# Kernel tuning notes

Measured on AMD Instinct MI355X. Metric: run time of the kernel, lower is better.

## Reference

```python
import jax, jax.numpy as jnp
import numpy as np

HIDDEN = 1024
FEAT = 64
BATCH = 512
SEQ = 64
EPS = 1e-5


def _gru_layer(x_seq, Wih, Whh, bih, bhh):
    # x_seq: [B,T,Din]; Wih: [3H,Din]; Whh: [3H,H]; gate order r,z,n (PyTorch)
    B = x_seq.shape[0]
    H = Whh.shape[1]
    gates_x = jnp.einsum('btd,gd->btg', x_seq, Wih) + bih  # [B,T,3H]
    h0 = jnp.zeros((B, H), x_seq.dtype)

    def step(h, gx):
        gh = h @ Whh.T + bhh                       # [B,3H]
        xr, xz, xn = jnp.split(gx, 3, axis=-1)
        hr, hz, hn = jnp.split(gh, 3, axis=-1)
        r = jax.nn.sigmoid(xr + hr)
        z = jax.nn.sigmoid(xz + hz)
        n = jnp.tanh(xn + r * hn)
        h_new = (1.0 - z) * n + z * h
        return h_new, h_new

    _, ys = jax.lax.scan(step, h0, jnp.swapaxes(gates_x, 0, 1))  # [T,B,H]
    return jnp.swapaxes(ys, 0, 1)                                # [B,T,H]


def setup_inputs() -> dict:
    key = jax.random.key(0)
    ks = jax.random.split(key, 20)
    s = 1.0 / np.sqrt(HIDDEN)
    u = lambda k, shape: jax.random.uniform(k, shape, jnp.float32, -s, s)
    inp = {
        'x': jax.random.normal(ks[0], (BATCH, SEQ, FEAT), jnp.float32),
        'Wih0': u(ks[1], (3 * HIDDEN, FEAT)),
        'Whh0': u(ks[2], (3 * HIDDEN, HIDDEN)),
        'bih0': u(ks[3], (3 * HIDDEN,)),
        'bhh0': u(ks[4], (3 * HIDDEN,)),
        'Wih1': u(ks[5], (3 * HIDDEN, HIDDEN)),
        'Whh1': u(ks[6], (3 * HIDDEN, HIDDEN)),
        'bih1': u(ks[7], (3 * HIDDEN,)),
        'bhh1': u(ks[8], (3 * HIDDEN,)),
        'Wih2': u(ks[9], (3 * HIDDEN, HIDDEN)),
        'Whh2': u(ks[10], (3 * HIDDEN, HIDDEN)),
        'bih2': u(ks[11], (3 * HIDDEN,)),
        'bhh2': u(ks[12], (3 * HIDDEN,)),
        'gamma': jnp.ones((HIDDEN,), jnp.float32),
        'beta': jnp.zeros((HIDDEN,), jnp.float32),
        'fcW': u(ks[13], (1, HIDDEN)),
        'fcb': u(ks[14], (1,)),
    }
    return inp


def reference(x, Wih0, Whh0, bih0, bhh0, Wih1, Whh1, bih1, bhh1,
              Wih2, Whh2, bih2, bhh2, gamma, beta, fcW, fcb):
    h = _gru_layer(x, Wih0, Whh0, bih0, bhh0)
    h = _gru_layer(h, Wih1, Whh1, bih1, bhh1)
    h = _gru_layer(h, Wih2, Whh2, bih2, bhh2)
    out = h[:, -1, :]                               # [B,H] last timestep
    # BatchNorm1d in training mode: biased batch stats (B != 1 branch)
    mu = jnp.mean(out, axis=0)
    var = jnp.mean((out - mu) ** 2, axis=0)
    out = (out - mu) * jax.lax.rsqrt(var + EPS) * gamma + beta
    out = out @ fcW.T + fcb                         # [B,1]
    return jax.nn.sigmoid(out)[:, 0]                # [B]
```

## Files before the change

kernel.cpp:

```cpp
#include <hip/hip_runtime.h>
#include <hip/hip_bf16.h>
#include <stdint.h>

#define HIDDEN 1024
#define FEAT   64
#define BATCH  512
#define SEQ    64
#define GATES  3072

typedef __attribute__((ext_vector_type(4))) float f32x4;
typedef __attribute__((ext_vector_type(8))) short s16x8;

#define MFMA16(a, b, c) __builtin_amdgcn_mfma_f32_16x16x32_bf16(a, b, c, 0, 0, 0)
#define VMCNT(n) asm volatile("s_waitcnt vmcnt(" #n ")" ::: "memory")
#define LGKMCNT0 asm volatile("s_waitcnt lgkmcnt(0)" ::: "memory")

__device__ inline unsigned short f2bf(float f) {
    unsigned u = __builtin_bit_cast(unsigned, f);
    u += 0x7fff + ((u >> 16) & 1);
    return (unsigned short)(u >> 16);
}
__device__ inline float bf2f(unsigned short s) {
    unsigned u = ((unsigned)s) << 16;
    return __builtin_bit_cast(float, u);
}

#define GLOAD_LDS16(g, l) __builtin_amdgcn_global_load_lds( \
    (const __attribute__((address_space(1))) unsigned int*)(g), \
    (__attribute__((address_space(3))) unsigned int*)(l), 16, 0, 0)

__global__ void k_conv_whh(const float* __restrict__ src, unsigned short* __restrict__ dst) {
    int i = blockIdx.x * 256 + threadIdx.x;
    int d = i >> 10, k = i & 1023;
    int ub = d / 48, rem = d - ub * 48;
    int g = rem >> 4, jj = rem & 15;
    int srow = g * 1024 + ub * 16 + jj;
    dst[i] = f2bf(src[(size_t)srow * 1024 + k]);
}

__global__ void k_conv_wih0(const float* __restrict__ src, unsigned short* __restrict__ dst) {
    int i = blockIdx.x * 256 + threadIdx.x;
    int d = i >> 6, k = i & 63;
    int ub = d / 48, rem = d - ub * 48;
    int g = rem >> 4, jj = rem & 15;
    int srow = g * 1024 + ub * 16 + jj;
    dst[i] = f2bf(src[(size_t)srow * 64 + k]);
}

__global__ void k_xpose(const float* __restrict__ x, unsigned short* __restrict__ xbf) {
    int i = blockIdx.x * blockDim.x + threadIdx.x;
    if (i >= BATCH * SEQ * FEAT) return;
    int f = i & 63, t = (i >> 6) & 63, b = i >> 12;
    xbf[((size_t)t * BATCH + b) * FEAT + f] = f2bf(x[i]);
}

__device__ __forceinline__ void stage_pair(const char* ws, int wstr, const char* as, int astr,
                                           unsigned short* Wd, unsigned short* Ad,
                                           int wid, int lane)
{
    const int lrow = lane >> 3;
    const int lcol = lane & 7;
    for (int g = wid; g < 6; g += 4) {
        int row = g * 8 + lrow;
        int c16 = lcol ^ (row & 7);
        GLOAD_LDS16(ws + (size_t)row * wstr + c16 * 16, (char*)Wd + (g << 10));
    }
#pragma unroll
    for (int r = 0; r < 4; ++r) {
        int g = wid + r * 4;
        int row = g * 8 + lrow;
        int c16 = lcol ^ (row & 7);
        GLOAD_LDS16(as + (size_t)row * astr + c16 * 16, (char*)Ad + (g << 10));
    }
}

template<int NSLOT>
__device__ __forceinline__ void compute_chunk(const unsigned short* aL, const unsigned short* wL,
                                              int wid, int lane, f32x4 (&acc)[2][4])
{
    const int l15 = lane & 15, hi = lane >> 4;
    const int swz = (l15 & 7) << 4;
    const char* ap = (const char*)aL;
    const char* wp = (const char*)wL;
#pragma unroll
    for (int ks = 0; ks < 2; ++ks) {
        const int kb = ks * 64 + (hi << 4);
        s16x8 a0 = *(const s16x8*)(ap + ((((wid * 32 + l15) * 128) + kb) ^ swz));
        s16x8 a1 = *(const s16x8*)(ap + ((((wid * 32 + 16 + l15) * 128) + kb) ^ swz));
        s16x8 b0 = *(const s16x8*)(wp + (((l15 * 128) + kb) ^ swz));
        s16x8 b1 = *(const s16x8*)(wp + ((((16 + l15) * 128) + kb) ^ swz));
        s16x8 b2 = *(const s16x8*)(wp + ((((32 + l15) * 128) + kb) ^ swz));
        acc[0][0]     = MFMA16(a0, b0, acc[0][0]);
        acc[0][1]     = MFMA16(a0, b1, acc[0][1]);
        acc[0][NSLOT] = MFMA16(a0, b2, acc[0][NSLOT]);
        acc[1][0]     = MFMA16(a1, b0, acc[1][0]);
        acc[1][1]     = MFMA16(a1, b1, acc[1][1]);
        acc[1][NSLOT] = MFMA16(a1, b2, acc[1][NSLOT]);
    }
}

__global__ __launch_bounds__(256, 3) void k_stage(
    int d,
    const unsigned short* __restrict__ xbf,
    unsigned short* __restrict__ h0,
    unsigned short* __restrict__ h1,
    unsigned short* __restrict__ h2,
    const unsigned short* __restrict__ wih0R,
    const unsigned short* __restrict__ whh0R,
    const unsigned short* __restrict__ wih1R,
    const unsigned short* __restrict__ whh1R,
    const unsigned short* __restrict__ wih2R,
    const unsigned short* __restrict__ whh2R,
    const float* __restrict__ bih0, const float* __restrict__ bhh0,
    const float* __restrict__ bih1, const float* __restrict__ bhh1,
    const float* __restrict__ bih2, const float* __restrict__ bhh2)
{
    __shared__ unsigned short Wb[2][48 * 64];
    __shared__ unsigned short Ab[2][128 * 64];
    const int bid = blockIdx.x;
    const int slot = bid & 7;
    const int p = (bid >> 3) % 24;
    const int bg = bid / 192;
    const int pair = slot + 8 * p;
    const int layer = pair >> 6;
    const int ub = pair & 63;
    const int t = d - layer;
    if (t < 0 || t >= SEQ) return;

    const int tid = threadIdx.x;
    const int wid = tid >> 6, lane = tid & 63;
    const int l15 = lane & 15, hi = lane >> 4;
    const int brow0 = bg * 128;

    const unsigned short* inseq = (layer == 0) ? xbf : ((layer == 1) ? h0 : h1);
    unsigned short* outseq = (layer == 0) ? h0 : ((layer == 1) ? h1 : h2);
    const unsigned short* wihR = (layer == 0) ? wih0R : ((layer == 1) ? wih1R : wih2R);
    const unsigned short* whhR = (layer == 0) ? whh0R : ((layer == 1) ? whh1R : whh2R);

    const int astr1 = (layer == 0) ? 128 : 2048;
    const char* a1base = (layer == 0)
        ? (const char*)xbf + (size_t)t * BATCH * FEAT * 2 + (size_t)brow0 * 128
        : (const char*)inseq + (size_t)t * BATCH * HIDDEN * 2 + (size_t)brow0 * 2048;
    const char* w1base = (layer == 0)
        ? (const char*)wihR + (size_t)ub * 48 * 64 * 2
        : (const char*)wihR + (size_t)ub * 48 * 1024 * 2;
    const int wstr1 = (layer == 0) ? 128 : 2048;
    const char* a2base = (const char*)outseq + (size_t)(t - 1) * BATCH * HIDDEN * 2 + (size_t)brow0 * 2048;
    const char* w2base = (const char*)whhR + (size_t)ub * 48 * 1024 * 2;

    const int NCH1 = (layer == 0) ? 1 : 16;
    const int NCH2 = (t > 0) ? 16 : 0;
    const int total = NCH1 + NCH2;

    auto srcs = [&](int c, const char*& ws, int& wstr, const char*& as, int& astr) {
        if (c < NCH1) {
            ws = w1base + (size_t)c * 128; wstr = wstr1;
            as = a1base + (size_t)c * 128; astr = astr1;
        } else {
            int c2 = c - NCH1;
            ws = w2base + (size_t)c2 * 128; wstr = 2048;
            as = a2base + (size_t)c2 * 128; astr = 2048;
        }
    };

    f32x4 acc[2][4];
    const f32x4 zero = {0.f, 0.f, 0.f, 0.f};
#pragma unroll
    for (int i = 0; i < 2; ++i)
#pragma unroll
        for (int s = 0; s < 4; ++s) acc[i][s] = zero;

    {
        const char* ws; int wstr; const char* as; int astr;
        srcs(0, ws, wstr, as, astr);
        stage_pair(ws, wstr, as, astr, Wb[0], Ab[0], wid, lane);
    }

    for (int c = 0; c < total; ++c) {
        const int cb = c & 1;
        if (c + 1 < total) {
            const char* ws; int wstr; const char* as; int astr;
            srcs(c + 1, ws, wstr, as, astr);
            stage_pair(ws, wstr, as, astr, Wb[cb ^ 1], Ab[cb ^ 1], wid, lane);
            if (wid < 2) VMCNT(6); else VMCNT(5);
        } else {
            VMCNT(0);
        }
        __builtin_amdgcn_s_barrier();
        __builtin_amdgcn_sched_barrier(0);
        if (c < NCH1) compute_chunk<2>(Ab[cb], Wb[cb], wid, lane, acc);
        else          compute_chunk<3>(Ab[cb], Wb[cb], wid, lane, acc);
        LGKMCNT0;
        __builtin_amdgcn_sched_barrier(0);
        __builtin_amdgcn_s_barrier();
    }

    const float* bih = (layer == 0) ? bih0 : ((layer == 1) ? bih1 : bih2);
    const float* bhh = (layer == 0) ? bhh0 : ((layer == 1) ? bhh1 : bhh2);
    const int j = ub * 16 + l15;
    const float br  = bih[j] + bhh[j];
    const float bz  = bih[HIDDEN + j] + bhh[HIDDEN + j];
    const float bxn = bih[2 * HIDDEN + j];
    const float bhn = bhh[2 * HIDDEN + j];
    const unsigned short* hprev = outseq + (size_t)((t > 0) ? (t - 1) : 0) * (BATCH * HIDDEN);
    unsigned short* hout = outseq + (size_t)t * (BATCH * HIDDEN);
#pragma unroll
    for (int i = 0; i < 2; ++i)
#pragma unroll
        for (int r = 0; r < 4; ++r) {
            int brow = brow0 + wid * 32 + i * 16 + hi * 4 + r;
            size_t hidx = (size_t)brow * HIDDEN + j;
            float rg = 1.f / (1.f + __expf(-(acc[i][0][r] + br)));
            float zg = 1.f / (1.f + __expf(-(acc[i][1][r] + bz)));
            float ng = tanhf(acc[i][2][r] + bxn + rg * (acc[i][3][r] + bhn));
            float hv = (t > 0) ? bf2f(hprev[hidx]) : 0.f;
            float hnew = (1.f - zg) * ng + zg * hv;
            hout[hidx] = f2bf(hnew);
        }
}

__global__ void k_bn_part(const unsigned short* __restrict__ h, float* __restrict__ part) {
    int j = threadIdx.x;
    int blk = blockIdx.x;
    float s = 0.f, q = 0.f;
    for (int b = blk * 32; b < blk * 32 + 32; ++b) {
        float v = bf2f(h[(size_t)b * HIDDEN + j]);
        s += v; q += v * v;
    }
    part[blk * 2048 + j] = s;
    part[blk * 2048 + 1024 + j] = q;
}

__global__ void k_bn_fold(const float* __restrict__ part, const float* __restrict__ gamma,
                          const float* __restrict__ beta, float* __restrict__ a, float* __restrict__ bb)
{
    int j = blockIdx.x * 256 + threadIdx.x;
    float s = 0.f, q = 0.f;
    for (int p = 0; p < 16; ++p) {
        s += part[p * 2048 + j];
        q += part[p * 2048 + 1024 + j];
    }
    float mu = s * (1.f / BATCH);
    float var = q * (1.f / BATCH) - mu * mu;
    float rs = rsqrtf(var + 1e-5f);
    float aj = gamma[j] * rs;
    a[j] = aj;
    bb[j] = beta[j] - mu * aj;
}

__global__ void k_fc(const unsigned short* __restrict__ h, const float* __restrict__ a, const float* __restrict__ bb,
                     const float* __restrict__ fcW, const float* __restrict__ fcb, float* __restrict__ out)
{
    int b = blockIdx.x;
    int lane = threadIdx.x;
    float s = 0.f;
    for (int j = lane; j < HIDDEN; j += 64)
        s += (bf2f(h[(size_t)b * HIDDEN + j]) * a[j] + bb[j]) * fcW[j];
#pragma unroll
    for (int m = 32; m; m >>= 1) s += __shfl_xor(s, m, 64);
    if (lane == 0) out[b] = 1.f / (1.f + __expf(-(s + fcb[0])));
}

extern "C" void kernel_launch(void* const* d_in, const int* in_sizes, int n_in,
                              void* d_out, int out_size, void* d_ws, size_t ws_size,
                              hipStream_t stream)
{
    const float* x = (const float*)d_in[0];
    const float* W_ih[3] = {(const float*)d_in[1], (const float*)d_in[5], (const float*)d_in[9]};
    const float* W_hh[3] = {(const float*)d_in[2], (const float*)d_in[6], (const float*)d_in[10]};
    const float* b_ih[3] = {(const float*)d_in[3], (const float*)d_in[7], (const float*)d_in[11]};
    const float* b_hh[3] = {(const float*)d_in[4], (const float*)d_in[8], (const float*)d_in[12]};
    const float* gamma = (const float*)d_in[13];
    const float* beta  = (const float*)d_in[14];
    const float* fcW   = (const float*)d_in[15];
    const float* fcb   = (const float*)d_in[16];

    char* ws = (char*)d_ws;
    size_t off = 0;
    auto alloc = [&](size_t bytes) -> void* {
        void* p = ws + off;
        off = (off + bytes + 255) & ~(size_t)255;
        return p;
    };
    unsigned short* wih0R = (unsigned short*)alloc((size_t)GATES * FEAT * 2);
    unsigned short* whh0R = (unsigned short*)alloc((size_t)GATES * HIDDEN * 2);
    unsigned short* wih1R = (unsigned short*)alloc((size_t)GATES * HIDDEN * 2);
    unsigned short* whh1R = (unsigned short*)alloc((size_t)GATES * HIDDEN * 2);
    unsigned short* wih2R = (unsigned short*)alloc((size_t)GATES * HIDDEN * 2);
    unsigned short* whh2R = (unsigned short*)alloc((size_t)GATES * HIDDEN * 2);
    unsigned short* xbf = (unsigned short*)alloc((size_t)SEQ * BATCH * FEAT * 2);
    unsigned short* h0  = (unsigned short*)alloc((size_t)SEQ * BATCH * HIDDEN * 2);
    unsigned short* h1  = (unsigned short*)alloc((size_t)SEQ * BATCH * HIDDEN * 2);
    unsigned short* h2  = (unsigned short*)alloc((size_t)SEQ * BATCH * HIDDEN * 2);
    float* part = (float*)alloc(16 * 2048 * 4);
    float* abuf = (float*)alloc(HIDDEN * 4);
    float* bbuf = (float*)alloc(HIDDEN * 4);

    k_conv_wih0<<<(GATES * FEAT) / 256, 256, 0, stream>>>(W_ih[0], wih0R);
    k_conv_whh<<<(GATES * HIDDEN) / 256, 256, 0, stream>>>(W_hh[0], whh0R);
    k_conv_whh<<<(GATES * HIDDEN) / 256, 256, 0, stream>>>(W_ih[1], wih1R);
    k_conv_whh<<<(GATES * HIDDEN) / 256, 256, 0, stream>>>(W_hh[1], whh1R);
    k_conv_whh<<<(GATES * HIDDEN) / 256, 256, 0, stream>>>(W_ih[2], wih2R);
    k_conv_whh<<<(GATES * HIDDEN) / 256, 256, 0, stream>>>(W_hh[2], whh2R);
    k_xpose<<<(BATCH * SEQ * FEAT + 255) / 256, 256, 0, stream>>>(x, xbf);

    for (int d = 0; d < SEQ + 2; ++d)
        k_stage<<<768, 256, 0, stream>>>(d, xbf, h0, h1, h2,
                                         wih0R, whh0R, wih1R, whh1R, wih2R, whh2R,
                                         b_ih[0], b_hh[0], b_ih[1], b_hh[1], b_ih[2], b_hh[2]);

    const unsigned short* hlast = h2 + (size_t)(SEQ - 1) * (BATCH * HIDDEN);
    k_bn_part<<<16, 1024, 0, stream>>>(hlast, part);
    k_bn_fold<<<HIDDEN / 256, 256, 0, stream>>>(part, gamma, beta, abuf, bbuf);
    k_fc<<<BATCH, 64, 0, stream>>>(hlast, abuf, bbuf, fcW, fcb, (float*)d_out);
}
```

Baseline: 2.323 ms.

## Tile weights and hidden states into contiguous 64-column chunks for staging

```diff
diff --git a/kernel.cpp b/kernel.cpp
--- a/kernel.cpp
+++ b/kernel.cpp
@@ -29,22 +29,24 @@
     (const __attribute__((address_space(1))) unsigned int*)(g), \
     (__attribute__((address_space(3))) unsigned int*)(l), 16, 0, 0)
 
-__global__ void k_conv_whh(const float* __restrict__ src, unsigned short* __restrict__ dst) {
+__global__ void k_conv_whh_t(const float* __restrict__ src, unsigned short* __restrict__ dst) {
     int i = blockIdx.x * 256 + threadIdx.x;
-    int d = i >> 10, k = i & 1023;
-    int ub = d / 48, rem = d - ub * 48;
-    int g = rem >> 4, jj = rem & 15;
-    int srow = g * 1024 + ub * 16 + jj;
-    dst[i] = f2bf(src[(size_t)srow * 1024 + k]);
-}
-
-__global__ void k_conv_wih0(const float* __restrict__ src, unsigned short* __restrict__ dst) {
+    int ub = i / 49152;
+    int r  = i - ub * 49152;
+    int c  = r / 3072;
+    int r2 = r - c * 3072;
+    int srow = r2 >> 6, scol = r2 & 63;
+    int src_row = ((srow >> 4) << 10) + (ub << 4) + (srow & 15);
+    dst[i] = f2bf(src[(size_t)src_row * 1024 + (c << 6) + scol]);
+}
+
+__global__ void k_conv_wih0_t(const float* __restrict__ src, unsigned short* __restrict__ dst) {
     int i = blockIdx.x * 256 + threadIdx.x;
-    int d = i >> 6, k = i & 63;
-    int ub = d / 48, rem = d - ub * 48;
-    int g = rem >> 4, jj = rem & 15;
-    int srow = g * 1024 + ub * 16 + jj;
-    dst[i] = f2bf(src[(size_t)srow * 64 + k]);
+    int ub = i / 3072;
+    int r  = i - ub * 3072;
+    int srow = r >> 6, scol = r & 63;
+    int src_row = ((srow >> 4) << 10) + (ub << 4) + (srow & 15);
+    dst[i] = f2bf(src[(size_t)src_row * 64 + scol]);
 }
 
 __global__ void k_xpose(const float* __restrict__ x, unsigned short* __restrict__ xbf) {
@@ -54,23 +56,18 @@
     xbf[((size_t)t * BATCH + b) * FEAT + f] = f2bf(x[i]);
 }
 
-__device__ __forceinline__ void stage_pair(const char* ws, int wstr, const char* as, int astr,
+__device__ __forceinline__ void stage_pair(const char* ws, const char* as,
                                            unsigned short* Wd, unsigned short* Ad,
                                            int wid, int lane)
 {
     const int lrow = lane >> 3;
-    const int lcol = lane & 7;
-    for (int g = wid; g < 6; g += 4) {
-        int row = g * 8 + lrow;
-        int c16 = lcol ^ (row & 7);
-        GLOAD_LDS16(ws + (size_t)row * wstr + c16 * 16, (char*)Wd + (g << 10));
-    }
+    const int srcoff = lrow * 128 + (((lane & 7) ^ (lrow & 7)) << 4);
+    for (int g = wid; g < 6; g += 4)
+        GLOAD_LDS16(ws + (g << 10) + srcoff, (char*)Wd + (g << 10));
 #pragma unroll
     for (int r = 0; r < 4; ++r) {
         int g = wid + r * 4;
-        int row = g * 8 + lrow;
-        int c16 = lcol ^ (row & 7);
-        GLOAD_LDS16(as + (size_t)row * astr + c16 * 16, (char*)Ad + (g << 10));
+        GLOAD_LDS16(as + (g << 10) + srcoff, (char*)Ad + (g << 10));
     }
 }
 
@@ -137,29 +134,27 @@
     const unsigned short* wihR = (layer == 0) ? wih0R : ((layer == 1) ? wih1R : wih2R);
     const unsigned short* whhR = (layer == 0) ? whh0R : ((layer == 1) ? whh1R : whh2R);
 
-    const int astr1 = (layer == 0) ? 128 : 2048;
     const char* a1base = (layer == 0)
-        ? (const char*)xbf + (size_t)t * BATCH * FEAT * 2 + (size_t)brow0 * 128
-        : (const char*)inseq + (size_t)t * BATCH * HIDDEN * 2 + (size_t)brow0 * 2048;
+        ? (const char*)xbf + (size_t)t * 65536 + (size_t)brow0 * 128
+        : (const char*)inseq + (size_t)t * 1048576 + (size_t)brow0 * 128;
     const char* w1base = (layer == 0)
-        ? (const char*)wihR + (size_t)ub * 48 * 64 * 2
-        : (const char*)wihR + (size_t)ub * 48 * 1024 * 2;
-    const int wstr1 = (layer == 0) ? 128 : 2048;
-    const char* a2base = (const char*)outseq + (size_t)(t - 1) * BATCH * HIDDEN * 2 + (size_t)brow0 * 2048;
-    const char* w2base = (const char*)whhR + (size_t)ub * 48 * 1024 * 2;
+        ? (const char*)wih0R + (size_t)ub * 6144
+        : (const char*)wihR + (size_t)ub * 98304;
+    const char* a2base = (const char*)outseq + (size_t)(t - 1) * 1048576 + (size_t)brow0 * 128;
+    const char* w2base = (const char*)whhR + (size_t)ub * 98304;
 
     const int NCH1 = (layer == 0) ? 1 : 16;
     const int NCH2 = (t > 0) ? 16 : 0;
     const int total = NCH1 + NCH2;
 
-    auto srcs = [&](int c, const char*& ws, int& wstr, const char*& as, int& astr) {
+    auto srcs = [&](int c, const char*& ws, const char*& as) {
         if (c < NCH1) {
-            ws = w1base + (size_t)c * 128; wstr = wstr1;
-            as = a1base + (size_t)c * 128; astr = astr1;
+            ws = w1base + (size_t)c * 6144;
+            as = a1base + (size_t)c * 65536;
         } else {
             int c2 = c - NCH1;
-            ws = w2base + (size_t)c2 * 128; wstr = 2048;
-            as = a2base + (size_t)c2 * 128; astr = 2048;
+            ws = w2base + (size_t)c2 * 6144;
+            as = a2base + (size_t)c2 * 65536;
         }
     };
 
@@ -171,17 +166,17 @@
         for (int s = 0; s < 4; ++s) acc[i][s] = zero;
 
     {
-        const char* ws; int wstr; const char* as; int astr;
-        srcs(0, ws, wstr, as, astr);
-        stage_pair(ws, wstr, as, astr, Wb[0], Ab[0], wid, lane);
+        const char* ws; const char* as;
+        srcs(0, ws, as);
+        stage_pair(ws, as, Wb[0], Ab[0], wid, lane);
     }
 
     for (int c = 0; c < total; ++c) {
         const int cb = c & 1;
         if (c + 1 < total) {
-            const char* ws; int wstr; const char* as; int astr;
-            srcs(c + 1, ws, wstr, as, astr);
-            stage_pair(ws, wstr, as, astr, Wb[cb ^ 1], Ab[cb ^ 1], wid, lane);
+            const char* ws; const char* as;
+            srcs(c + 1, ws, as);
+            stage_pair(ws, as, Wb[cb ^ 1], Ab[cb ^ 1], wid, lane);
             if (wid < 2) VMCNT(6); else VMCNT(5);
         } else {
             VMCNT(0);
@@ -202,14 +197,16 @@
     const float bz  = bih[HIDDEN + j] + bhh[HIDDEN + j];
     const float bxn = bih[2 * HIDDEN + j];
     const float bhn = bhh[2 * HIDDEN + j];
-    const unsigned short* hprev = outseq + (size_t)((t > 0) ? (t - 1) : 0) * (BATCH * HIDDEN);
-    unsigned short* hout = outseq + (size_t)t * (BATCH * HIDDEN);
+    const unsigned short* hprev = outseq + (size_t)((t > 0) ? (t - 1) : 0) * (16 * 512 * 64);
+    unsigned short* hout = outseq + (size_t)t * (16 * 512 * 64);
+    const int jc = (ub >> 2);
+    const int jcol = (ub & 3) * 16 + l15;
 #pragma unroll
     for (int i = 0; i < 2; ++i)
 #pragma unroll
         for (int r = 0; r < 4; ++r) {
             int brow = brow0 + wid * 32 + i * 16 + hi * 4 + r;
-            size_t hidx = (size_t)brow * HIDDEN + j;
+            size_t hidx = (size_t)(jc * 512 + brow) * 64 + jcol;
             float rg = 1.f / (1.f + __expf(-(acc[i][0][r] + br)));
             float zg = 1.f / (1.f + __expf(-(acc[i][1][r] + bz)));
             float ng = tanhf(acc[i][2][r] + bxn + rg * (acc[i][3][r] + bhn));
@@ -222,9 +219,10 @@
 __global__ void k_bn_part(const unsigned short* __restrict__ h, float* __restrict__ part) {
     int j = threadIdx.x;
     int blk = blockIdx.x;
+    const int jc = j >> 6, jcol = j & 63;
     float s = 0.f, q = 0.f;
     for (int b = blk * 32; b < blk * 32 + 32; ++b) {
-        float v = bf2f(h[(size_t)b * HIDDEN + j]);
+        float v = bf2f(h[(size_t)(jc * 512 + b) * 64 + jcol]);
         s += v; q += v * v;
     }
     part[blk * 2048 + j] = s;
@@ -255,7 +253,7 @@
     int lane = threadIdx.x;
     float s = 0.f;
     for (int j = lane; j < HIDDEN; j += 64)
-        s += (bf2f(h[(size_t)b * HIDDEN + j]) * a[j] + bb[j]) * fcW[j];
+        s += (bf2f(h[(size_t)((j >> 6) * 512 + b) * 64 + (j & 63)]) * a[j] + bb[j]) * fcW[j];
 #pragma unroll
     for (int m = 32; m; m >>= 1) s += __shfl_xor(s, m, 64);
     if (lane == 0) out[b] = 1.f / (1.f + __expf(-(s + fcb[0])));
@@ -296,12 +294,12 @@
     float* abuf = (float*)alloc(HIDDEN * 4);
     float* bbuf = (float*)alloc(HIDDEN * 4);
 
-    k_conv_wih0<<<(GATES * FEAT) / 256, 256, 0, stream>>>(W_ih[0], wih0R);
-    k_conv_whh<<<(GATES * HIDDEN) / 256, 256, 0, stream>>>(W_hh[0], whh0R);
-    k_conv_whh<<<(GATES * HIDDEN) / 256, 256, 0, stream>>>(W_ih[1], wih1R);
-    k_conv_whh<<<(GATES * HIDDEN) / 256, 256, 0, stream>>>(W_hh[1], whh1R);
-    k_conv_whh<<<(GATES * HIDDEN) / 256, 256, 0, stream>>>(W_ih[2], wih2R);
-    k_conv_whh<<<(GATES * HIDDEN) / 256, 256, 0, stream>>>(W_hh[2], whh2R);
+    k_conv_wih0_t<<<(GATES * FEAT) / 256, 256, 0, stream>>>(W_ih[0], wih0R);
+    k_conv_whh_t<<<(GATES * HIDDEN) / 256, 256, 0, stream>>>(W_hh[0], whh0R);
+    k_conv_whh_t<<<(GATES * HIDDEN) / 256, 256, 0, stream>>>(W_ih[1], wih1R);
+    k_conv_whh_t<<<(GATES * HIDDEN) / 256, 256, 0, stream>>>(W_hh[1], whh1R);
+    k_conv_whh_t<<<(GATES * HIDDEN) / 256, 256, 0, stream>>>(W_ih[2], wih2R);
+    k_conv_whh_t<<<(GATES * HIDDEN) / 256, 256, 0, stream>>>(W_hh[2], whh2R);
     k_xpose<<<(BATCH * SEQ * FEAT + 255) / 256, 256, 0, stream>>>(x, xbf);
 
     for (int d = 0; d < SEQ + 2; ++d)
```

New measurement: 2.204 ms. 1.05x faster.
